# Performance work log

Measured on AMD Instinct MI355X. Metric: run time of the kernel, lower is better.

Reference implementation:

```python
import jax, jax.numpy as jnp
import numpy as np

DT = 0.02          # full control timestep (cfg dt)
N_SUBSTEPS = 8     # RK4 substeps per forward call
LMBDA = 0.5        # first-order actuator lag gain
G_VEC = jnp.array([0.0, 0.0, -9.81], dtype=jnp.float32)
N_ENVS = 2097152


def setup_inputs() -> dict:
    key = jax.random.key(0)
    k1, k2 = jax.random.split(key)
    X0 = jax.random.normal(k1, (N_ENVS, 9), dtype=jnp.float32)
    U = jax.random.normal(k2, (N_ENVS, 3), dtype=jnp.float32)
    return {"X0": X0, "U": U}


def reference(X0, U):
    h = DT / N_SUBSTEPS  # substep size

    def dynamics(X):
        v = X[:, 3:6]
        a = X[:, 6:9]
        a_dot = LMBDA * (U - a) / DT   # actuator lag uses full dt, as in torch code
        # X_dot = [p_dot, v_dot, a_dot] = [v, a - g_vec, a_dot]
        return jnp.concatenate([v, a - G_VEC, a_dot], axis=-1)

    def rk4_step(X, _):
        k1 = dynamics(X)
        k2 = dynamics(X + 0.5 * h * k1)
        k3 = dynamics(X + 0.5 * h * k2)
        k4 = dynamics(X + h * k3)
        X_next = X + (h / 6.0) * (k1 + 2.0 * k2 + 2.0 * k3 + k4)
        return X_next, None

    X_final, _ = jax.lax.scan(rk4_step, X0, None, length=N_SUBSTEPS)
    return X_final
```

## Files before the change

### kernel.cpp

```cpp
#include <hip/hip_runtime.h>


#define ENVS_PER_BLOCK 256
#define THREADS 256

struct Coeffs {
    float P00, P01, P02;
    float P10, P11, P12;
    float P20, P21, P22;
    float Ku0, Ku1, Ku2;
    float Kg0, Kg1, Kg2;
};

__global__ __launch_bounds__(THREADS)
void pointmass_kernel(const float* __restrict__ X0,
                      const float* __restrict__ U,
                      float* __restrict__ Out,
                      int envTotal, Coeffs cf) {
    __shared__ float s_x[ENVS_PER_BLOCK * 9];
    __shared__ float s_u[ENVS_PER_BLOCK * 3];

    const int t = threadIdx.x;
    const int blockBase = blockIdx.x * ENVS_PER_BLOCK;
    const int envsHere = min(ENVS_PER_BLOCK, envTotal - blockBase);

    if (envsHere == ENVS_PER_BLOCK) {
        const float4* x4 = (const float4*)(X0 + (size_t)blockBase * 9);
        const float4* u4 = (const float4*)(U  + (size_t)blockBase * 3);
        float4* o4 = (float4*)(Out + (size_t)blockBase * 9);

        #pragma unroll
        for (int j = t; j < ENVS_PER_BLOCK * 9 / 4; j += THREADS)
            ((float4*)s_x)[j] = x4[j];
        if (t < ENVS_PER_BLOCK * 3 / 4)
            ((float4*)s_u)[t] = u4[t];
        __syncthreads();

        float r[9];
        #pragma unroll
        for (int k = 0; k < 3; ++k) {
            const float p = s_x[t * 9 + k];
            const float v = s_x[t * 9 + 3 + k];
            const float a = s_x[t * 9 + 6 + k];
            const float u = s_u[t * 3 + k];
            const float g = (k == 2) ? -9.81f : 0.0f;
            r[k]     = cf.P00 * p + cf.P01 * v + cf.P02 * a + cf.Ku0 * u + cf.Kg0 * g;
            r[3 + k] = cf.P10 * p + cf.P11 * v + cf.P12 * a + cf.Ku1 * u + cf.Kg1 * g;
            r[6 + k] = cf.P20 * p + cf.P21 * v + cf.P22 * a + cf.Ku2 * u + cf.Kg2 * g;
        }
        #pragma unroll
        for (int i = 0; i < 9; ++i) s_x[t * 9 + i] = r[i];
        __syncthreads();

        #pragma unroll
        for (int j = t; j < ENVS_PER_BLOCK * 9 / 4; j += THREADS)
            o4[j] = ((const float4*)s_x)[j];
    } else {
        for (int j = t; j < envsHere * 9; j += THREADS)
            s_x[j] = X0[(size_t)blockBase * 9 + j];
        for (int j = t; j < envsHere * 3; j += THREADS)
            s_u[j] = U[(size_t)blockBase * 3 + j];
        __syncthreads();
        if (t < envsHere) {
            float r[9];
            #pragma unroll
            for (int k = 0; k < 3; ++k) {
                const float p = s_x[t * 9 + k];
                const float v = s_x[t * 9 + 3 + k];
                const float a = s_x[t * 9 + 6 + k];
                const float u = s_u[t * 3 + k];
                const float g = (k == 2) ? -9.81f : 0.0f;
                r[k]     = cf.P00 * p + cf.P01 * v + cf.P02 * a + cf.Ku0 * u + cf.Kg0 * g;
                r[3 + k] = cf.P10 * p + cf.P11 * v + cf.P12 * a + cf.Ku1 * u + cf.Kg1 * g;
                r[6 + k] = cf.P20 * p + cf.P21 * v + cf.P22 * a + cf.Ku2 * u + cf.Kg2 * g;
            }
            #pragma unroll
            for (int i = 0; i < 9; ++i)
                Out[((size_t)blockBase + t) * 9 + i] = r[i];
        }
    }
}

static void mat3_mul(const double A[3][3], const double B[3][3], double C[3][3]) {
    for (int i = 0; i < 3; ++i)
        for (int j = 0; j < 3; ++j) {
            double s = 0.0;
            for (int k = 0; k < 3; ++k) s += A[i][k] * B[k][j];
            C[i][j] = s;
        }
}
static void mat3_copy(const double A[3][3], double B[3][3]) {
    for (int i = 0; i < 3; ++i) for (int j = 0; j < 3; ++j) B[i][j] = A[i][j];
}

extern "C" void kernel_launch(void* const* d_in, const int* in_sizes, int n_in,
                              void* d_out, int out_size, void* d_ws, size_t ws_size,
                              hipStream_t stream) {
    const float* X0 = (const float*)d_in[0];
    const float* U  = (const float*)d_in[1];
    float* Out = (float*)d_out;
    const int envTotal = in_sizes[0] / 9;

    const double DT = 0.02;
    const double h = DT / 8.0;
    const double c = 0.5 / DT;
    double hA[3][3] = {{0, h, 0}, {0, 0, h}, {0, 0, -c * h}};

    double hA2[3][3], hA3[3][3], hA4[3][3];
    mat3_mul(hA, hA, hA2);
    mat3_mul(hA2, hA, hA3);
    mat3_mul(hA3, hA, hA4);

    double P[3][3], Q[3][3];
    for (int i = 0; i < 3; ++i)
        for (int j = 0; j < 3; ++j) {
            const double I = (i == j) ? 1.0 : 0.0;
            P[i][j] = I + hA[i][j] + hA2[i][j] / 2.0 + hA3[i][j] / 6.0 + hA4[i][j] / 24.0;
            Q[i][j] = h * (I + hA[i][j] / 2.0 + hA2[i][j] / 6.0 + hA3[i][j] / 24.0);
        }

    double P2[3][3], P4[3][3], P8[3][3];
    mat3_mul(P, P, P2);
    mat3_mul(P2, P2, P4);
    mat3_mul(P4, P4, P8);

    double IP[3][3], IP2[3][3], IP4[3][3], T[3][3], S[3][3], R[3][3];
    mat3_copy(P, IP);  mat3_copy(P2, IP2);  mat3_copy(P4, IP4);
    for (int i = 0; i < 3; ++i) { IP[i][i] += 1.0; IP2[i][i] += 1.0; IP4[i][i] += 1.0; }
    mat3_mul(IP, IP2, T);
    mat3_mul(T, IP4, S);
    mat3_mul(S, Q, R);

    Coeffs cf;
    cf.P00 = (float)P8[0][0]; cf.P01 = (float)P8[0][1]; cf.P02 = (float)P8[0][2];
    cf.P10 = (float)P8[1][0]; cf.P11 = (float)P8[1][1]; cf.P12 = (float)P8[1][2];
    cf.P20 = (float)P8[2][0]; cf.P21 = (float)P8[2][1]; cf.P22 = (float)P8[2][2];
    cf.Ku0 = (float)(R[0][2] * c); cf.Ku1 = (float)(R[1][2] * c); cf.Ku2 = (float)(R[2][2] * c);
    cf.Kg0 = (float)(-R[0][1]);    cf.Kg1 = (float)(-R[1][1]);    cf.Kg2 = (float)(-R[2][1]);

    const int blocks = (envTotal + ENVS_PER_BLOCK - 1) / ENVS_PER_BLOCK;
    pointmass_kernel<<<blocks, THREADS, 0, stream>>>(X0, U, Out, envTotal, cf);
}
```

Measured before the change: 153.2 us.

## Process four envs per thread with direct float4 loads, dropping LDS staging

Each thread now handles four consecutive environments, loading 9 float4 of state and 3 float4 of control directly into registers and writing 9 float4 back, instead of staging a block's data through shared memory with two barriers. The gravity term is folded into a precomputed per-row constant added only to the z component. This removes LDS traffic and synchronisation, but each thread's float4 accesses are strided by 144 bytes across lanes, so global access coalescing is worse and the grid has a quarter as many threads.

After: 180.1 us. 17.6% more time.

```diff
diff --git a/kernel.cpp b/kernel.cpp
--- a/kernel.cpp
+++ b/kernel.cpp
@@ -1,7 +1,6 @@
 #include <hip/hip_runtime.h>
 
 
-#define ENVS_PER_BLOCK 256
 #define THREADS 256
 
 struct Coeffs {
@@ -9,7 +8,7 @@
     float P10, P11, P12;
     float P20, P21, P22;
     float Ku0, Ku1, Ku2;
-    float Kg0, Kg1, Kg2;
+    float G0,  G1,  G2;
 };
 
 __global__ __launch_bounds__(THREADS)
@@ -17,66 +16,63 @@
                       const float* __restrict__ U,
                       float* __restrict__ Out,
                       int envTotal, Coeffs cf) {
-    __shared__ float s_x[ENVS_PER_BLOCK * 9];
-    __shared__ float s_u[ENVS_PER_BLOCK * 3];
+    const int tid = blockIdx.x * THREADS + threadIdx.x;
+    const int envBase = tid * 4;
+    if (envBase >= envTotal) return;
 
-    const int t = threadIdx.x;
-    const int blockBase = blockIdx.x * ENVS_PER_BLOCK;
-    const int envsHere = min(ENVS_PER_BLOCK, envTotal - blockBase);
+    if (envBase + 4 <= envTotal) {
+        const float4* x4 = (const float4*)(X0 + (size_t)envBase * 9);
+        const float4* u4 = (const float4*)(U  + (size_t)envBase * 3);
+        float4*       o4 = (float4*)(Out + (size_t)envBase * 9);
 
-    if (envsHere == ENVS_PER_BLOCK) {
-        const float4* x4 = (const float4*)(X0 + (size_t)blockBase * 9);
-        const float4* u4 = (const float4*)(U  + (size_t)blockBase * 3);
-        float4* o4 = (float4*)(Out + (size_t)blockBase * 9);
+        float4 xin[9], uin[3], oo[9];
+        #pragma unroll
+        for (int j = 0; j < 9; ++j) xin[j] = x4[j];
+        #pragma unroll
+        for (int j = 0; j < 3; ++j) uin[j] = u4[j];
+
+        const float* x = (const float*)xin;
+        const float* u = (const float*)uin;
+        float*       o = (float*)oo;
 
         #pragma unroll
-        for (int j = t; j < ENVS_PER_BLOCK * 9 / 4; j += THREADS)
-            ((float4*)s_x)[j] = x4[j];
-        if (t < ENVS_PER_BLOCK * 3 / 4)
-            ((float4*)s_u)[t] = u4[t];
-        __syncthreads();
-
-        float r[9];
-        #pragma unroll
-        for (int k = 0; k < 3; ++k) {
-            const float p = s_x[t * 9 + k];
-            const float v = s_x[t * 9 + 3 + k];
-            const float a = s_x[t * 9 + 6 + k];
-            const float u = s_u[t * 3 + k];
-            const float g = (k == 2) ? -9.81f : 0.0f;
-            r[k]     = cf.P00 * p + cf.P01 * v + cf.P02 * a + cf.Ku0 * u + cf.Kg0 * g;
-            r[3 + k] = cf.P10 * p + cf.P11 * v + cf.P12 * a + cf.Ku1 * u + cf.Kg1 * g;
-            r[6 + k] = cf.P20 * p + cf.P21 * v + cf.P22 * a + cf.Ku2 * u + cf.Kg2 * g;
+        for (int m = 0; m < 4; ++m) {
+            #pragma unroll
+            for (int k = 0; k < 3; ++k) {
+                const float p  = x[9 * m + k];
+                const float v  = x[9 * m + 3 + k];
+                const float a  = x[9 * m + 6 + k];
+                const float uu = u[3 * m + k];
+                float r0 = cf.P00 * p + cf.P01 * v + cf.P02 * a + cf.Ku0 * uu;
+                float r1 = cf.P10 * p + cf.P11 * v + cf.P12 * a + cf.Ku1 * uu;
+                float r2 = cf.P20 * p + cf.P21 * v + cf.P22 * a + cf.Ku2 * uu;
+                if (k == 2) { r0 += cf.G0; r1 += cf.G1; r2 += cf.G2; }
+                o[9 * m + k]     = r0;
+                o[9 * m + 3 + k] = r1;
+                o[9 * m + 6 + k] = r2;
+            }
         }
-        #pragma unroll
-        for (int i = 0; i < 9; ++i) s_x[t * 9 + i] = r[i];
-        __syncthreads();
 
         #pragma unroll
-        for (int j = t; j < ENVS_PER_BLOCK * 9 / 4; j += THREADS)
-            o4[j] = ((const float4*)s_x)[j];
+        for (int j = 0; j < 9; ++j) o4[j] = oo[j];
     } else {
-        for (int j = t; j < envsHere * 9; j += THREADS)
-            s_x[j] = X0[(size_t)blockBase * 9 + j];
-        for (int j = t; j < envsHere * 3; j += THREADS)
-            s_u[j] = U[(size_t)blockBase * 3 + j];
-        __syncthreads();
-        if (t < envsHere) {
-            float r[9];
-            #pragma unroll
+        for (int e = envBase; e < envTotal; ++e) {
+            float p[3], v[3], a[3], uu[3];
             for (int k = 0; k < 3; ++k) {
-                const float p = s_x[t * 9 + k];
-                const float v = s_x[t * 9 + 3 + k];
-                const float a = s_x[t * 9 + 6 + k];
-                const float u = s_u[t * 3 + k];
-                const float g = (k == 2) ? -9.81f : 0.0f;
-                r[k]     = cf.P00 * p + cf.P01 * v + cf.P02 * a + cf.Ku0 * u + cf.Kg0 * g;
-                r[3 + k] = cf.P10 * p + cf.P11 * v + cf.P12 * a + cf.Ku1 * u + cf.Kg1 * g;
-                r[6 + k] = cf.P20 * p + cf.P21 * v + cf.P22 * a + cf.Ku2 * u + cf.Kg2 * g;
+                p[k]  = X0[(size_t)e * 9 + k];
+                v[k]  = X0[(size_t)e * 9 + 3 + k];
+                a[k]  = X0[(size_t)e * 9 + 6 + k];
+                uu[k] = U[(size_t)e * 3 + k];
             }
-            #pragma unroll
-            for (int i = 0; i < 9; ++i)
-                Out[((size_t)blockBase + t) * 9 + i] = r[i];
+            for (int k = 0; k < 3; ++k) {
+                float r0 = cf.P00 * p[k] + cf.P01 * v[k] + cf.P02 * a[k] + cf.Ku0 * uu[k];
+                float r1 = cf.P10 * p[k] + cf.P11 * v[k] + cf.P12 * a[k] + cf.Ku1 * uu[k];
+                float r2 = cf.P20 * p[k] + cf.P21 * v[k] + cf.P22 * a[k] + cf.Ku2 * uu[k];
+                if (k == 2) { r0 += cf.G0; r1 += cf.G1; r2 += cf.G2; }
+                Out[(size_t)e * 9 + k]     = r0;
+                Out[(size_t)e * 9 + 3 + k] = r1;
+                Out[(size_t)e * 9 + 6 + k] = r2;
+            }
         }
     }
 }
@@ -136,8 +132,11 @@
     cf.P10 = (float)P8[1][0]; cf.P11 = (float)P8[1][1]; cf.P12 = (float)P8[1][2];
     cf.P20 = (float)P8[2][0]; cf.P21 = (float)P8[2][1]; cf.P22 = (float)P8[2][2];
     cf.Ku0 = (float)(R[0][2] * c); cf.Ku1 = (float)(R[1][2] * c); cf.Ku2 = (float)(R[2][2] * c);
-    cf.Kg0 = (float)(-R[0][1]);    cf.Kg1 = (float)(-R[1][1]);    cf.Kg2 = (float)(-R[2][1]);
+    cf.G0 = (float)(R[0][1] * 9.81);
+    cf.G1 = (float)(R[1][1] * 9.81);
+    cf.G2 = (float)(R[2][1] * 9.81);
 
-    const int blocks = (envTotal + ENVS_PER_BLOCK - 1) / ENVS_PER_BLOCK;
+    const int nThreads = (envTotal + 3) / 4;
+    const int blocks = (nThreads + THREADS - 1) / THREADS;
     pointmass_kernel<<<blocks, THREADS, 0, stream>>>(X0, U, Out, envTotal, cf);
 }
```
